# Performance work log

Measured on AMD Instinct MI355X. Metric: run time of the kernel, lower is better.

## Reference

```python
import jax, jax.numpy as jnp
import numpy as np

B, C, H, W = 2, 128, 96, 96
HEADS, DHEAD, WIN = 4, 32, 5
INNER = HEADS * DHEAD
PAD = WIN // 2


def setup_inputs() -> dict:
    key = jax.random.key(0)
    k1, k2, k3, k4, k5 = jax.random.split(key, 5)
    s = 1.0 / np.sqrt(C)
    return {
        "x": jax.random.normal(k1, (B, C, H, W), dtype=jnp.float32),
        "wq": jax.random.normal(k2, (INNER, C), dtype=jnp.float32) * s,
        "wk": jax.random.normal(k3, (INNER, C), dtype=jnp.float32) * s,
        "wv": jax.random.normal(k4, (INNER, C), dtype=jnp.float32) * s,
        "wproj": jax.random.normal(k5, (C, INNER), dtype=jnp.float32) * s,
    }


def _windows(t):
    # same neighborhood ordering as F.unfold (row-major over kernel offsets).
    tp = jnp.pad(t, ((0, 0), (0, 0), (0, 0), (PAD, PAD), (PAD, PAD)))
    wins = [tp[:, :, :, di:di + H, dj:dj + W]
            for di in range(WIN) for dj in range(WIN)]
    return jnp.stack(wins, axis=3)


def reference(x, wq, wk, wv, wproj):
    # 1x1 convs == per-pixel linear maps
    q = jnp.einsum('oc,bcxy->boxy', wq, x).reshape(B, HEADS, DHEAD, H, W)
    k = jnp.einsum('oc,bcxy->boxy', wk, x).reshape(B, HEADS, DHEAD, H, W)
    v = jnp.einsum('oc,bcxy->boxy', wv, x).reshape(B, HEADS, DHEAD, H, W)

    k_win = _windows(k)  # (B,h,d,25,H,W)
    v_win = _windows(v)

    scale = 1.0 / np.sqrt(DHEAD)
    attn = jnp.einsum('bhdxy,bhdkxy->bhkxy', q, k_win) * scale
    attn = jax.nn.softmax(attn, axis=2)  # softmax over the 25 window positions
    out = jnp.einsum('bhkxy,bhdkxy->bhdxy', attn, v_win)

    out = out.reshape(B, INNER, H, W)
    return jnp.einsum('co,boxy->bcxy', wproj, out)
```

## Files before the change

### kernel.cpp

```cpp
#include <hip/hip_runtime.h>
#include <hip/hip_bf16.h>
#include <hip/hip_fp16.h>

#define PP 9216
#define OO 384

typedef _Float16 f16x8 __attribute__((ext_vector_type(8)));
typedef _Float16 h2    __attribute__((ext_vector_type(2)));
typedef float    f32x4 __attribute__((ext_vector_type(4)));

#if defined(__has_builtin)
# if __has_builtin(__builtin_amdgcn_fdot2)
#  define HAS_FDOT2 1
# endif
#endif

__device__ __forceinline__ float dot2acc(h2 a, h2 b, float c) {
#ifdef HAS_FDOT2
    return __builtin_amdgcn_fdot2(a, b, c, false);
#else
    return c + (float)a[0] * (float)b[0] + (float)a[1] * (float)b[1];
#endif
}

__device__ __forceinline__ f16x8 cvt8(float4 u0, float4 u1) {
    f16x8 r;
    r[0] = (_Float16)u0.x; r[1] = (_Float16)u0.y;
    r[2] = (_Float16)u0.z; r[3] = (_Float16)u0.w;
    r[4] = (_Float16)u1.x; r[5] = (_Float16)u1.y;
    r[6] = (_Float16)u1.z; r[7] = (_Float16)u1.w;
    return r;
}

__global__ __launch_bounds__(256) void qkv_gemm(
    const float* __restrict__ x, const float* __restrict__ wq,
    const float* __restrict__ wk, const float* __restrict__ wv,
    _Float16* __restrict__ qkv)
{
    __shared__ _Float16 sEpi[4][32][104];

    const int b = blockIdx.z;
    const int p0 = blockIdx.x * 64;
    const int nbase = blockIdx.y * 192;
    const int t = threadIdx.x;
    const int w = t >> 6, lane = t & 63;
    const int lm = lane & 15, quad = lane >> 4;
    const int ms0 = (w & 1) * 32;
    const int nw = (w >> 1) * 96;

    const float* xb = x + (size_t)b * 128 * PP;
    _Float16* qb = qkv + (size_t)b * PP * OO;

    f16x8 A[2][4];
    #pragma unroll
    for (int ms = 0; ms < 2; ms++) {
        const float* xp = xb + p0 + ms0 + ms * 16 + lm;
        #pragma unroll
        for (int kc = 0; kc < 4; kc++) {
            const float* s = xp + (size_t)(kc * 32 + quad * 8) * PP;
            float tmp[8];
            #pragma unroll
            for (int j = 0; j < 8; j++) tmp[j] = s[(size_t)j * PP];
            #pragma unroll
            for (int j = 0; j < 8; j++) A[ms][kc][j] = (_Float16)tmp[j];
        }
    }

    for (int nt = 0; nt < 6; nt++) {
        const int n0 = nbase + nw + nt * 16;
        const int o = n0 + lm;
        const float* wrow = (o < 128) ? (wq + (size_t)o * 128)
                          : (o < 256) ? (wk + (size_t)(o - 128) * 128)
                                      : (wv + (size_t)(o - 256) * 128);
        f16x8 Bf[4];
        #pragma unroll
        for (int kc = 0; kc < 4; kc++) {
            float4 u0 = *(const float4*)(wrow + kc * 32 + quad * 8);
            float4 u1 = *(const float4*)(wrow + kc * 32 + quad * 8 + 4);
            Bf[kc] = cvt8(u0, u1);
        }
        f32x4 acc[2];
        #pragma unroll
        for (int ms = 0; ms < 2; ms++) {
            acc[ms] = (f32x4){0.f, 0.f, 0.f, 0.f};
            #pragma unroll
            for (int kc = 0; kc < 4; kc++)
                acc[ms] = __builtin_amdgcn_mfma_f32_16x16x32_f16(A[ms][kc], Bf[kc], acc[ms], 0, 0, 0);
        }
        #pragma unroll
        for (int ms = 0; ms < 2; ms++)
            #pragma unroll
            for (int r = 0; r < 4; r++)
                sEpi[w][ms * 16 + quad * 4 + r][nt * 16 + lm] = (_Float16)acc[ms][r];
    }

    #pragma unroll
    for (int it = 0; it < 6; it++) {
        int idx = it * 64 + lane;
        int row = idx / 12;
        int ch  = idx % 12;
        uint4 v = *(const uint4*)&sEpi[w][row][ch * 8];
        *(uint4*)(qb + (size_t)(p0 + ms0 + row) * OO + nbase + nw + ch * 8) = v;
    }
}

__global__ __launch_bounds__(256) void attn2(
    const _Float16* __restrict__ qkv, _Float16* __restrict__ ao)
{
    __shared__ _Float16 sK[144 * 40];
    __shared__ _Float16 sV[144 * 40];
    __shared__ float sS[64 * 27];

    const int t = threadIdx.x;
    const int x0 = blockIdx.x * 8, y0 = blockIdx.y * 8;
    const int b = blockIdx.z >> 2, h = blockIdx.z & 3;
    const _Float16* base = qkv + (size_t)b * PP * OO;

    for (int u = t; u < 288; u += 256) {
        const int arr = (u >= 144) ? 1 : 0;
        const int pos = u - 144 * arr;
        const int gy = y0 - 2 + pos / 12;
        const int gx = x0 - 2 + pos % 12;
        _Float16* dst = (arr ? sV : sK) + pos * 40;
        if ((unsigned)gy < 96u && (unsigned)gx < 96u) {
            const _Float16* src = base + (size_t)(gy * 96 + gx) * OO + 128 + arr * 128 + h * 32;
            #pragma unroll
            for (int j = 0; j < 4; j++)
                *(uint4*)(dst + j * 8) = *(const uint4*)(src + j * 8);
        } else {
            uint4 z = {0u, 0u, 0u, 0u};
            #pragma unroll
            for (int j = 0; j < 4; j++) *(uint4*)(dst + j * 8) = z;
        }
    }

    const int px = t & 63, w = t >> 6;
    const int ly = px >> 3, lx = px & 7;
    const int gp = (y0 + ly) * 96 + x0 + lx;

    h2 qreg[16];
    {
        const _Float16* qs = base + (size_t)gp * OO + h * 32;
        #pragma unroll
        for (int j = 0; j < 4; j++)
            *(uint4*)(&qreg[j * 4]) = *(const uint4*)(qs + j * 8);
    }
    __syncthreads();

    const float scale = 0.17677669529663689f;
    for (int pos = w; pos < 25; pos += 4) {
        const int hp = (ly + pos / 5) * 12 + lx + pos % 5;
        const _Float16* kr = sK + hp * 40;
        h2 kreg[16];
        #pragma unroll
        for (int j = 0; j < 4; j++)
            *(uint4*)(&kreg[j * 4]) = *(const uint4*)(kr + j * 8);
        float s0 = 0.f, s1 = 0.f;
        #pragma unroll
        for (int j = 0; j < 8; j++) {
            s0 = dot2acc(qreg[2 * j], kreg[2 * j], s0);
            s1 = dot2acc(qreg[2 * j + 1], kreg[2 * j + 1], s1);
        }
        sS[px * 27 + pos] = (s0 + s1) * scale;
    }
    __syncthreads();

    if ((t & 63) < 16) {
        const int sp = (t >> 6) * 16 + (t & 15);
        float* row = sS + sp * 27;
        float m = row[0];
        #pragma unroll
        for (int p = 1; p < 25; p++) m = fmaxf(m, row[p]);
        float sum = 0.f;
        float e[25];
        #pragma unroll
        for (int p = 0; p < 25; p++) { e[p] = __expf(row[p] - m); sum += e[p]; }
        const float inv = 1.f / sum;
        #pragma unroll
        for (int p = 0; p < 25; p++) row[p] = e[p] * inv;
    }
    __syncthreads();

    float at[25];
    #pragma unroll
    for (int p = 0; p < 25; p++) at[p] = sS[px * 27 + p];

    float f[8];
    #pragma unroll
    for (int j = 0; j < 8; j++) f[j] = 0.f;
    for (int p = 0; p < 25; p++) {
        const int hp = (ly + p / 5) * 12 + lx + p % 5;
        h2 vreg[4];
        *(uint4*)vreg = *(const uint4*)(sV + hp * 40 + w * 8);
        #pragma unroll
        for (int j = 0; j < 4; j++) {
            f[2 * j]     += at[p] * (float)vreg[j][0];
            f[2 * j + 1] += at[p] * (float)vreg[j][1];
        }
    }
    _Float16 ho[8];
    #pragma unroll
    for (int j = 0; j < 8; j++) ho[j] = (_Float16)f[j];
    *(uint4*)(ao + ((size_t)b * PP + gp) * 128 + h * 32 + w * 8) = *(uint4*)ho;
}

__global__ __launch_bounds__(256) void proj_gemm(
    const _Float16* __restrict__ ao, const float* __restrict__ wp,
    float* __restrict__ out)
{
    const int b = blockIdx.z;
    const int p0 = blockIdx.x * 32;
    const int t = threadIdx.x;
    const int w = t >> 6, lane = t & 63;
    const int lm = lane & 15, quad = lane >> 4;
    const int ms0 = (w & 1) * 16;
    const int nw = (w >> 1) * 64;

    const _Float16* ab = ao + (size_t)b * PP * 128;
    float* ob = out + (size_t)b * 128 * PP;

    f16x8 A[4];
    #pragma unroll
    for (int kc = 0; kc < 4; kc++)
        A[kc] = *(const f16x8*)(ab + (size_t)(p0 + ms0 + lm) * 128 + kc * 32 + quad * 8);

    #pragma unroll
    for (int nt = 0; nt < 4; nt++) {
        const int n0 = nw + nt * 16;
        const float* wrow = wp + (size_t)(n0 + lm) * 128;
        f16x8 Bf[4];
        #pragma unroll
        for (int kc = 0; kc < 4; kc++) {
            float4 u0 = *(const float4*)(wrow + kc * 32 + quad * 8);
            float4 u1 = *(const float4*)(wrow + kc * 32 + quad * 8 + 4);
            Bf[kc] = cvt8(u0, u1);
        }
        f32x4 acc = (f32x4){0.f, 0.f, 0.f, 0.f};
        #pragma unroll
        for (int kc = 0; kc < 4; kc++)
            acc = __builtin_amdgcn_mfma_f32_16x16x32_f16(A[kc], Bf[kc], acc, 0, 0, 0);
        float4 v = make_float4(acc[0], acc[1], acc[2], acc[3]);
        *(float4*)(ob + (size_t)(n0 + lm) * PP + p0 + ms0 + quad * 4) = v;
    }
}

extern "C" void kernel_launch(void* const* d_in, const int* in_sizes, int n_in,
                              void* d_out, int out_size, void* d_ws, size_t ws_size,
                              hipStream_t stream)
{
    const float* x  = (const float*)d_in[0];
    const float* wq = (const float*)d_in[1];
    const float* wk = (const float*)d_in[2];
    const float* wv = (const float*)d_in[3];
    const float* wp = (const float*)d_in[4];
    float* out = (float*)d_out;

    _Float16* qkvh = (_Float16*)d_ws;
    _Float16* aoh  = qkvh + 7077888;

    qkv_gemm<<<dim3(144, 2, 2), 256, 0, stream>>>(x, wq, wk, wv, qkvh);
    attn2<<<dim3(12, 12, 8), 256, 0, stream>>>(qkvh, aoh);
    proj_gemm<<<dim3(288, 1, 2), 256, 0, stream>>>(aoh, wp, out);
}
```

Before: 118.6 us.

## Fuse QKV projection, neighborhood attention and output projection into one kernel

Replaces the three kernels (QKV GEMM, windowed attention, projection GEMM) with one kernel per 8x8 spatial tile that keeps everything in LDS. K and V are recomputed for the 12x12 halo tile and Q for the inner tile. Scores are computed as a dense 64x144 MFMA product and then gathered to the 25 window positions, and P·V uses MFMA over a zero-filled probability matrix. This removes the global round trip of the qkv and attention-output intermediates and two launches. In exchange it does redundant halo K/V work and wasted dense MFMA work, and uses about 156KB of LDS, which limits it to one block per CU.

```diff
diff --git a/kernel.cpp b/kernel.cpp
--- a/kernel.cpp
+++ b/kernel.cpp
@@ -1,27 +1,22 @@
 #include <hip/hip_runtime.h>
-#include <hip/hip_bf16.h>
 #include <hip/hip_fp16.h>
 
 #define PP 9216
-#define OO 384
 
 typedef _Float16 f16x8 __attribute__((ext_vector_type(8)));
-typedef _Float16 h2    __attribute__((ext_vector_type(2)));
+typedef _Float16 f16x4 __attribute__((ext_vector_type(4)));
 typedef float    f32x4 __attribute__((ext_vector_type(4)));
 
-#if defined(__has_builtin)
-# if __has_builtin(__builtin_amdgcn_fdot2)
-#  define HAS_FDOT2 1
-# endif
-#endif
-
-__device__ __forceinline__ float dot2acc(h2 a, h2 b, float c) {
-#ifdef HAS_FDOT2
-    return __builtin_amdgcn_fdot2(a, b, c, false);
-#else
-    return c + (float)a[0] * (float)b[0] + (float)a[1] * (float)b[1];
-#endif
-}
+#define SXW 136
+#define SVW 168
+#define SSW 145
+
+#define OFF_A   0
+#define OFF_K   39168
+#define OFF_VT  78336
+#define OFF_Q   121344
+#define OFF_AO  138752
+#define LDS_BYTES 156160
 
 __device__ __forceinline__ f16x8 cvt8(float4 u0, float4 u1) {
     f16x8 r;
@@ -32,215 +27,221 @@
     return r;
 }
 
-__global__ __launch_bounds__(256) void qkv_gemm(
-    const float* __restrict__ x, const float* __restrict__ wq,
+__global__ __launch_bounds__(256) void fused_attn(
+    const float* __restrict__ x,  const float* __restrict__ wq,
     const float* __restrict__ wk, const float* __restrict__ wv,
-    _Float16* __restrict__ qkv)
+    const float* __restrict__ wp, float* __restrict__ out)
 {
-    __shared__ _Float16 sEpi[4][32][104];
-
-    const int b = blockIdx.z;
-    const int p0 = blockIdx.x * 64;
-    const int nbase = blockIdx.y * 192;
+    __shared__ __align__(16) char smem[LDS_BYTES];
+    __shared__ float sInv[64];
+    _Float16* sX  = (_Float16*)(smem + OFF_A);
+    float*    sS  = (float*)   (smem + OFF_A);
+    _Float16* sP  = (_Float16*)(smem + OFF_A);
+    _Float16* sK  = (_Float16*)(smem + OFF_K);
+    _Float16* sVT = (_Float16*)(smem + OFF_VT);
+    _Float16* sQ  = (_Float16*)(smem + OFF_Q);
+    _Float16* sAo = (_Float16*)(smem + OFF_AO);
+
     const int t = threadIdx.x;
-    const int w = t >> 6, lane = t & 63;
-    const int lm = lane & 15, quad = lane >> 4;
-    const int ms0 = (w & 1) * 32;
-    const int nw = (w >> 1) * 96;
-
+    const int w = t >> 6, lane = t & 63, lm = lane & 15, quad = lane >> 4;
+    const int x0 = blockIdx.x * 8, y0 = blockIdx.y * 8, b = blockIdx.z;
     const float* xb = x + (size_t)b * 128 * PP;
-    _Float16* qb = qkv + (size_t)b * PP * OO;
-
-    f16x8 A[2][4];
+    float* ob = out + (size_t)b * 128 * PP;
+
+    #pragma unroll 4
+    for (int i = 0; i < 72; i++) {
+        int e = i * 256 + t;
+        int c = e / 144, pos = e - c * 144;
+        int hy = pos / 12, hx = pos - hy * 12;
+        int gy = y0 - 2 + hy, gx = x0 - 2 + hx;
+        float v = 0.f;
+        if ((unsigned)gy < 96u && (unsigned)gx < 96u)
+            v = xb[(size_t)c * PP + gy * 96 + gx];
+        sX[pos * SXW + c] = (_Float16)v;
+    }
+    if (t < 128) {
+        f16x4 z4 = {(_Float16)0, (_Float16)0, (_Float16)0, (_Float16)0};
+        #pragma unroll
+        for (int j = 0; j < 24; j += 4)
+            *(f16x4*)(sVT + t * SVW + 144 + j) = z4;
+    }
+
+    f16x8 BKV[4][4];
     #pragma unroll
-    for (int ms = 0; ms < 2; ms++) {
-        const float* xp = xb + p0 + ms0 + ms * 16 + lm;
-        #pragma unroll
-        for (int kc = 0; kc < 4; kc++) {
-            const float* s = xp + (size_t)(kc * 32 + quad * 8) * PP;
-            float tmp[8];
-            #pragma unroll
-            for (int j = 0; j < 8; j++) tmp[j] = s[(size_t)j * PP];
-            #pragma unroll
-            for (int j = 0; j < 8; j++) A[ms][kc][j] = (_Float16)tmp[j];
-        }
-    }
-
-    for (int nt = 0; nt < 6; nt++) {
-        const int n0 = nbase + nw + nt * 16;
-        const int o = n0 + lm;
-        const float* wrow = (o < 128) ? (wq + (size_t)o * 128)
-                          : (o < 256) ? (wk + (size_t)(o - 128) * 128)
-                                      : (wv + (size_t)(o - 256) * 128);
-        f16x8 Bf[4];
-        #pragma unroll
-        for (int kc = 0; kc < 4; kc++) {
-            float4 u0 = *(const float4*)(wrow + kc * 32 + quad * 8);
-            float4 u1 = *(const float4*)(wrow + kc * 32 + quad * 8 + 4);
-            Bf[kc] = cvt8(u0, u1);
-        }
-        f32x4 acc[2];
-        #pragma unroll
-        for (int ms = 0; ms < 2; ms++) {
-            acc[ms] = (f32x4){0.f, 0.f, 0.f, 0.f};
+    for (int ni = 0; ni < 4; ni++) {
+        int n = w + 4 * ni;
+        const float* wr = (ni < 2) ? (wk + (size_t)(n * 16 + lm) * 128)
+                                   : (wv + (size_t)((n - 8) * 16 + lm) * 128);
+        #pragma unroll
+        for (int kc = 0; kc < 4; kc++)
+            BKV[ni][kc] = cvt8(*(const float4*)(wr + kc * 32 + quad * 8),
+                               *(const float4*)(wr + kc * 32 + quad * 8 + 4));
+    }
+    __syncthreads();
+
+    for (int m = 0; m < 9; m++) {
+        f16x8 A[4];
+        #pragma unroll
+        for (int kc = 0; kc < 4; kc++)
+            A[kc] = *(const f16x8*)(sX + (m * 16 + lm) * SXW + kc * 32 + quad * 8);
+        #pragma unroll
+        for (int ni = 0; ni < 4; ni++) {
+            f32x4 acc = {0.f, 0.f, 0.f, 0.f};
             #pragma unroll
             for (int kc = 0; kc < 4; kc++)
-                acc[ms] = __builtin_amdgcn_mfma_f32_16x16x32_f16(A[ms][kc], Bf[kc], acc[ms], 0, 0, 0);
-        }
-        #pragma unroll
-        for (int ms = 0; ms < 2; ms++)
+                acc = __builtin_amdgcn_mfma_f32_16x16x32_f16(A[kc], BKV[ni][kc], acc, 0, 0, 0);
+            int n = w + 4 * ni;
+            if (ni < 2) {
+                #pragma unroll
+                for (int r = 0; r < 4; r++)
+                    sK[(m * 16 + quad * 4 + r) * SXW + n * 16 + lm] = (_Float16)acc[r];
+            } else {
+                f16x4 tv;
+                #pragma unroll
+                for (int r = 0; r < 4; r++) tv[r] = (_Float16)acc[r];
+                *(f16x4*)(sVT + ((n - 8) * 16 + lm) * SVW + m * 16 + quad * 4) = tv;
+            }
+        }
+    }
+
+    {
+        int qpx = w * 16 + lm;
+        int hrow = ((qpx >> 3) + 2) * 12 + (qpx & 7) + 2;
+        f16x8 A[4];
+        #pragma unroll
+        for (int kc = 0; kc < 4; kc++)
+            A[kc] = *(const f16x8*)(sX + hrow * SXW + kc * 32 + quad * 8);
+        for (int n = 0; n < 8; n++) {
+            const float* wr = wq + (size_t)(n * 16 + lm) * 128;
+            f32x4 acc = {0.f, 0.f, 0.f, 0.f};
+            #pragma unroll
+            for (int kc = 0; kc < 4; kc++) {
+                f16x8 Bf = cvt8(*(const float4*)(wr + kc * 32 + quad * 8),
+                                *(const float4*)(wr + kc * 32 + quad * 8 + 4));
+                acc = __builtin_amdgcn_mfma_f32_16x16x32_f16(A[kc], Bf, acc, 0, 0, 0);
+            }
             #pragma unroll
             for (int r = 0; r < 4; r++)
-                sEpi[w][ms * 16 + quad * 4 + r][nt * 16 + lm] = (_Float16)acc[ms][r];
-    }
-
-    #pragma unroll
-    for (int it = 0; it < 6; it++) {
-        int idx = it * 64 + lane;
-        int row = idx / 12;
-        int ch  = idx % 12;
-        uint4 v = *(const uint4*)&sEpi[w][row][ch * 8];
-        *(uint4*)(qb + (size_t)(p0 + ms0 + row) * OO + nbase + nw + ch * 8) = v;
-    }
-}
-
-__global__ __launch_bounds__(256) void attn2(
-    const _Float16* __restrict__ qkv, _Float16* __restrict__ ao)
-{
-    __shared__ _Float16 sK[144 * 40];
-    __shared__ _Float16 sV[144 * 40];
-    __shared__ float sS[64 * 27];
-
-    const int t = threadIdx.x;
-    const int x0 = blockIdx.x * 8, y0 = blockIdx.y * 8;
-    const int b = blockIdx.z >> 2, h = blockIdx.z & 3;
-    const _Float16* base = qkv + (size_t)b * PP * OO;
-
-    for (int u = t; u < 288; u += 256) {
-        const int arr = (u >= 144) ? 1 : 0;
-        const int pos = u - 144 * arr;
-        const int gy = y0 - 2 + pos / 12;
-        const int gx = x0 - 2 + pos % 12;
-        _Float16* dst = (arr ? sV : sK) + pos * 40;
-        if ((unsigned)gy < 96u && (unsigned)gx < 96u) {
-            const _Float16* src = base + (size_t)(gy * 96 + gx) * OO + 128 + arr * 128 + h * 32;
-            #pragma unroll
-            for (int j = 0; j < 4; j++)
-                *(uint4*)(dst + j * 8) = *(const uint4*)(src + j * 8);
-        } else {
-            uint4 z = {0u, 0u, 0u, 0u};
-            #pragma unroll
-            for (int j = 0; j < 4; j++) *(uint4*)(dst + j * 8) = z;
-        }
-    }
-
-    const int px = t & 63, w = t >> 6;
+                sQ[(w * 16 + quad * 4 + r) * SXW + n * 16 + lm] = (_Float16)acc[r];
+        }
+    }
+    __syncthreads();
+
+    const int px = lane;
     const int ly = px >> 3, lx = px & 7;
-    const int gp = (y0 + ly) * 96 + x0 + lx;
-
-    h2 qreg[16];
+
+    for (int h = 0; h < 4; h++) {
+        {
+            f16x8 A[4];
+            #pragma unroll
+            for (int m = 0; m < 4; m++)
+                A[m] = *(const f16x8*)(sQ + (m * 16 + lm) * SXW + h * 32 + quad * 8);
+            #pragma unroll
+            for (int ni = 0; ni < 3; ni++) {
+                int n = w + 4 * ni;
+                if (n < 9) {
+                    f16x8 B = *(const f16x8*)(sK + (n * 16 + lm) * SXW + h * 32 + quad * 8);
+                    #pragma unroll
+                    for (int m = 0; m < 4; m++) {
+                        f32x4 acc = {0.f, 0.f, 0.f, 0.f};
+                        acc = __builtin_amdgcn_mfma_f32_16x16x32_f16(A[m], B, acc, 0, 0, 0);
+                        #pragma unroll
+                        for (int r = 0; r < 4; r++)
+                            sS[(m * 16 + quad * 4 + r) * SSW + n * 16 + lm] = acc[r];
+                    }
+                }
+            }
+        }
+        __syncthreads();
+
+        float ev[25]; float inv;
+        {
+            const float scale = 0.17677669529663689f;
+            float sv[25];
+            #pragma unroll
+            for (int p = 0; p < 25; p++) {
+                int hp = (ly + p / 5) * 12 + lx + p % 5;
+                sv[p] = sS[px * SSW + hp] * scale;
+            }
+            float mx = sv[0];
+            #pragma unroll
+            for (int p = 1; p < 25; p++) mx = fmaxf(mx, sv[p]);
+            float sum = 0.f;
+            #pragma unroll
+            for (int p = 0; p < 25; p++) { ev[p] = __expf(sv[p] - mx); sum += ev[p]; }
+            inv = 1.f / sum;
+            if (w == 0) sInv[px] = inv;
+        }
+        __syncthreads();
+
+        {
+            _Float16* pr = sP + px * SVW;
+            const int s0 = w * 40, s1 = (w == 3) ? SVW : (w * 40 + 40);
+            f16x4 z4 = {(_Float16)0, (_Float16)0, (_Float16)0, (_Float16)0};
+            for (int cb = s0; cb < s1; cb += 4)
+                *(f16x4*)(pr + cb) = z4;
+            #pragma unroll
+            for (int p = 0; p < 25; p++) {
+                int hp = (ly + p / 5) * 12 + lx + p % 5;
+                if (hp >= s0 && hp < s1) pr[hp] = (_Float16)ev[p];
+            }
+        }
+        __syncthreads();
+
+        {
+            f16x8 A[5];
+            #pragma unroll
+            for (int k5 = 0; k5 < 5; k5++)
+                A[k5] = *(const f16x8*)(sP + (w * 16 + lm) * SVW + k5 * 32 + quad * 8);
+            float ivr[4];
+            *(float4*)ivr = *(const float4*)(sInv + w * 16 + quad * 4);
+            #pragma unroll
+            for (int n = 0; n < 2; n++) {
+                f32x4 acc = {0.f, 0.f, 0.f, 0.f};
+                #pragma unroll
+                for (int k5 = 0; k5 < 5; k5++) {
+                    f16x8 B = *(const f16x8*)(sVT + (h * 32 + n * 16 + lm) * SVW + k5 * 32 + quad * 8);
+                    acc = __builtin_amdgcn_mfma_f32_16x16x32_f16(A[k5], B, acc, 0, 0, 0);
+                }
+                #pragma unroll
+                for (int r = 0; r < 4; r++)
+                    sAo[(w * 16 + quad * 4 + r) * SXW + h * 32 + n * 16 + lm] =
+                        (_Float16)(acc[r] * ivr[r]);
+            }
+        }
+        __syncthreads();
+    }
+
     {
-        const _Float16* qs = base + (size_t)gp * OO + h * 32;
-        #pragma unroll
-        for (int j = 0; j < 4; j++)
-            *(uint4*)(&qreg[j * 4]) = *(const uint4*)(qs + j * 8);
-    }
-    __syncthreads();
-
-    const float scale = 0.17677669529663689f;
-    for (int pos = w; pos < 25; pos += 4) {
-        const int hp = (ly + pos / 5) * 12 + lx + pos % 5;
-        const _Float16* kr = sK + hp * 40;
-        h2 kreg[16];
-        #pragma unroll
-        for (int j = 0; j < 4; j++)
-            *(uint4*)(&kreg[j * 4]) = *(const uint4*)(kr + j * 8);
-        float s0 = 0.f, s1 = 0.f;
-        #pragma unroll
-        for (int j = 0; j < 8; j++) {
-            s0 = dot2acc(qreg[2 * j], kreg[2 * j], s0);
-            s1 = dot2acc(qreg[2 * j + 1], kreg[2 * j + 1], s1);
-        }
-        sS[px * 27 + pos] = (s0 + s1) * scale;
-    }
-    __syncthreads();
-
-    if ((t & 63) < 16) {
-        const int sp = (t >> 6) * 16 + (t & 15);
-        float* row = sS + sp * 27;
-        float m = row[0];
-        #pragma unroll
-        for (int p = 1; p < 25; p++) m = fmaxf(m, row[p]);
-        float sum = 0.f;
-        float e[25];
-        #pragma unroll
-        for (int p = 0; p < 25; p++) { e[p] = __expf(row[p] - m); sum += e[p]; }
-        const float inv = 1.f / sum;
-        #pragma unroll
-        for (int p = 0; p < 25; p++) row[p] = e[p] * inv;
-    }
-    __syncthreads();
-
-    float at[25];
-    #pragma unroll
-    for (int p = 0; p < 25; p++) at[p] = sS[px * 27 + p];
-
-    float f[8];
-    #pragma unroll
-    for (int j = 0; j < 8; j++) f[j] = 0.f;
-    for (int p = 0; p < 25; p++) {
-        const int hp = (ly + p / 5) * 12 + lx + p % 5;
-        h2 vreg[4];
-        *(uint4*)vreg = *(const uint4*)(sV + hp * 40 + w * 8);
-        #pragma unroll
-        for (int j = 0; j < 4; j++) {
-            f[2 * j]     += at[p] * (float)vreg[j][0];
-            f[2 * j + 1] += at[p] * (float)vreg[j][1];
-        }
-    }
-    _Float16 ho[8];
-    #pragma unroll
-    for (int j = 0; j < 8; j++) ho[j] = (_Float16)f[j];
-    *(uint4*)(ao + ((size_t)b * PP + gp) * 128 + h * 32 + w * 8) = *(uint4*)ho;
-}
-
-__global__ __launch_bounds__(256) void proj_gemm(
-    const _Float16* __restrict__ ao, const float* __restrict__ wp,
-    float* __restrict__ out)
-{
-    const int b = blockIdx.z;
-    const int p0 = blockIdx.x * 32;
-    const int t = threadIdx.x;
-    const int w = t >> 6, lane = t & 63;
-    const int lm = lane & 15, quad = lane >> 4;
-    const int ms0 = (w & 1) * 16;
-    const int nw = (w >> 1) * 64;
-
-    const _Float16* ab = ao + (size_t)b * PP * 128;
-    float* ob = out + (size_t)b * 128 * PP;
-
-    f16x8 A[4];
-    #pragma unroll
-    for (int kc = 0; kc < 4; kc++)
-        A[kc] = *(const f16x8*)(ab + (size_t)(p0 + ms0 + lm) * 128 + kc * 32 + quad * 8);
-
-    #pragma unroll
-    for (int nt = 0; nt < 4; nt++) {
-        const int n0 = nw + nt * 16;
-        const float* wrow = wp + (size_t)(n0 + lm) * 128;
-        f16x8 Bf[4];
-        #pragma unroll
-        for (int kc = 0; kc < 4; kc++) {
-            float4 u0 = *(const float4*)(wrow + kc * 32 + quad * 8);
-            float4 u1 = *(const float4*)(wrow + kc * 32 + quad * 8 + 4);
-            Bf[kc] = cvt8(u0, u1);
-        }
-        f32x4 acc = (f32x4){0.f, 0.f, 0.f, 0.f};
-        #pragma unroll
-        for (int kc = 0; kc < 4; kc++)
-            acc = __builtin_amdgcn_mfma_f32_16x16x32_f16(A[kc], Bf[kc], acc, 0, 0, 0);
-        float4 v = make_float4(acc[0], acc[1], acc[2], acc[3]);
-        *(float4*)(ob + (size_t)(n0 + lm) * PP + p0 + ms0 + quad * 4) = v;
+        f16x8 Aw[2][4];
+        #pragma unroll
+        for (int mi = 0; mi < 2; mi++) {
+            const float* wr = wp + (size_t)((w * 2 + mi) * 16 + lm) * 128;
+            #pragma unroll
+            for (int kc = 0; kc < 4; kc++)
+                Aw[mi][kc] = cvt8(*(const float4*)(wr + kc * 32 + quad * 8),
+                                  *(const float4*)(wr + kc * 32 + quad * 8 + 4));
+        }
+        #pragma unroll
+        for (int n = 0; n < 4; n++) {
+            f16x8 Bf[4];
+            #pragma unroll
+            for (int kc = 0; kc < 4; kc++)
+                Bf[kc] = *(const f16x8*)(sAo + (n * 16 + lm) * SXW + kc * 32 + quad * 8);
+            int pxc = n * 16 + lm;
+            int gp = (y0 + (pxc >> 3)) * 96 + x0 + (pxc & 7);
+            #pragma unroll
+            for (int mi = 0; mi < 2; mi++) {
+                f32x4 acc = {0.f, 0.f, 0.f, 0.f};
+                #pragma unroll
+                for (int kc = 0; kc < 4; kc++)
+                    acc = __builtin_amdgcn_mfma_f32_16x16x32_f16(Aw[mi][kc], Bf[kc], acc, 0, 0, 0);
+                int c0 = (w * 2 + mi) * 16 + quad * 4;
+                #pragma unroll
+                for (int r = 0; r < 4; r++)
+                    ob[(size_t)(c0 + r) * PP + gp] = acc[r];
+            }
+        }
     }
 }
 
@@ -255,10 +256,5 @@
     const float* wp = (const float*)d_in[4];
     float* out = (float*)d_out;
 
-    _Float16* qkvh = (_Float16*)d_ws;
-    _Float16* aoh  = qkvh + 7077888;
-
-    qkv_gemm<<<dim3(144, 2, 2), 256, 0, stream>>>(x, wq, wk, wv, qkvh);
-    attn2<<<dim3(12, 12, 8), 256, 0, stream>>>(qkvh, aoh);
-    proj_gemm<<<dim3(288, 1, 2), 256, 0, stream>>>(aoh, wp, out);
+    fused_attn<<<dim3(12, 12, 2), 256, 0, stream>>>(x, wq, wk, wv, wp, out);
 }
```

Result: slower. 163.4 us (+37.8%).
